# Kernel tuning notes

Measured on AMD Instinct MI355X. Metric: run time of the kernel, lower is better.

The kernel has to match this reference:

```python
import jax, jax.numpy as jnp
import numpy as np

NUM_HEAD = 16
EMBED_DIM = 1024
HEAD_DIM = EMBED_DIM // NUM_HEAD
QK_DIM = EMBED_DIM  # qk_dim defaults to embed_dim


def setup_inputs() -> dict:
    key = jax.random.key(0)
    k1, k2, k3 = jax.random.split(key, 3)
    x = jax.random.normal(k1, (4, 2048, EMBED_DIM), dtype=jnp.float32)
    # xavier_uniform-like init scale
    lim_qkv = float(np.sqrt(6.0 / (EMBED_DIM + 3 * EMBED_DIM)))
    lim_out = float(np.sqrt(6.0 / (EMBED_DIM + EMBED_DIM)))
    W_QKV = jax.random.uniform(k2, (EMBED_DIM, 3 * EMBED_DIM), jnp.float32, -lim_qkv, lim_qkv)
    W_Out = jax.random.uniform(k3, (EMBED_DIM, EMBED_DIM), jnp.float32, -lim_out, lim_out)
    return {"x": x, "W_QKV": W_QKV, "W_Out": W_Out}


def reference(x, W_QKV, W_Out):
    bsz, slen, _ = x.shape
    # [b,s,3E] -> [b,s,H,hd,3] -> [b,H,s,hd,3]  (interleaved qkv layout, as in torch source)
    qkv = (x @ W_QKV).reshape(bsz, slen, NUM_HEAD, HEAD_DIM, 3).transpose(0, 2, 1, 3, 4)
    q, k, v = qkv[..., 0], qkv[..., 1], qkv[..., 2]
    # NOTE: module scales by sqrt(qk_dim) (full dim), not sqrt(head_dim)
    scores = jnp.einsum("bhqd,bhkd->bhqk", q, k) / np.sqrt(QK_DIM).astype(np.float32)
    attn = jax.nn.softmax(scores, axis=-1)  # dropout p=0.0 -> identity
    out = jnp.einsum("bhqk,bhkd->bhqd", attn, v)  # [b,H,s,hd]
    out = out.transpose(0, 2, 1, 3).reshape(bsz, slen, EMBED_DIM)
    return out @ W_Out
```

## Files before the change

kernel.cpp:

```cpp
#include <hip/hip_runtime.h>
#include <stdint.h>

typedef __bf16 bf16x8 __attribute__((ext_vector_type(8)));
typedef float f32x4 __attribute__((ext_vector_type(4)));
typedef float f32x16 __attribute__((ext_vector_type(16)));
typedef unsigned short u16x8 __attribute__((ext_vector_type(8)));

#if __has_builtin(__builtin_amdgcn_mfma_f32_32x32x16_bf16)
#define MFMA32(a, b, c) __builtin_amdgcn_mfma_f32_32x32x16_bf16((a), (b), (c), 0, 0, 0)
#else
static __device__ __forceinline__ f32x16 MFMA32(bf16x8, bf16x8, f32x16 c) { return c; }
#endif

#if __has_builtin(__builtin_amdgcn_exp2f)
#define EXP2(x) __builtin_amdgcn_exp2f(x)
#else
#define EXP2(x) exp2f(x)
#endif

#if __has_builtin(__builtin_amdgcn_s_setprio)
#define SETPRIO(n) __builtin_amdgcn_s_setprio(n)
#else
#define SETPRIO(n)
#endif

__device__ __forceinline__ unsigned short f2bf(float f) {
    unsigned int u = __float_as_uint(f);
    u += 0x7fffu + ((u >> 16) & 1u);
    return (unsigned short)(u >> 16);
}

__device__ __forceinline__ int swz64(int row, int c) {
    return (c & 7) | ((((c >> 3) ^ row) & 7) << 3);
}

__device__ __forceinline__ int vperm32(int d, int s) {
    int c8 = ((s >> 5) << 2) | (((s >> 4) & 1) << 1) | ((s >> 2) & 1);
    int intra = (s & 3) | (((s >> 3) & 1) << 2);
    return intra + (((c8 ^ d) & 7) << 3);
}

__device__ __forceinline__ void glds16(const unsigned short* g, unsigned short* l) {
    __builtin_amdgcn_global_load_lds((const __attribute__((address_space(1))) void*)g,
                                     (__attribute__((address_space(3))) void*)l, 16, 0, 0);
}

__device__ __forceinline__ void transpose_body(const float* __restrict__ in,
                                               unsigned short* __restrict__ out,
                                               unsigned short (*tile)[33],
                                               int K, int N, int permute, int nb, int kb) {
    int tx = threadIdx.x & 31, ty = threadIdx.x >> 5;
    #pragma unroll
    for (int r = ty; r < 32; r += 8)
        tile[r][tx] = f2bf(in[(size_t)(kb + r) * N + nb + tx]);
    __syncthreads();
    #pragma unroll
    for (int r = ty; r < 32; r += 8) {
        int n_orig = nb + r, col = kb + tx;
        int row;
        if (permute) {
            int h = n_orig / 192, rem = n_orig - h * 192;
            int d = rem / 3, cc = rem - 3 * d;
            row = cc * 1024 + h * 64 + d;
        } else {
            row = n_orig;
        }
        out[(size_t)row * K + (col & ~63) + swz64(row, col & 63)] = tile[tx][r];
    }
}

__global__ __launch_bounds__(256) void preprocess_kernel(const float* __restrict__ x,
                                                         const float* __restrict__ wqkv,
                                                         const float* __restrict__ wout,
                                                         unsigned short* __restrict__ xb,
                                                         unsigned short* __restrict__ wqkvt,
                                                         unsigned short* __restrict__ woutt) {
    __shared__ unsigned short tile[32][33];
    int bid = blockIdx.x;
    if (bid < 4096) {
        size_t id = (size_t)bid * 256 + threadIdx.x;
        int row = (int)(id >> 7);
        int cid = (int)(id & 127);
        const float4* src = (const float4*)(x + id * 8);
        float4 a = src[0], b = src[1];
        u16x8 o;
        o[0] = f2bf(a.x); o[1] = f2bf(a.y); o[2] = f2bf(a.z); o[3] = f2bf(a.w);
        o[4] = f2bf(b.x); o[5] = f2bf(b.y); o[6] = f2bf(b.z); o[7] = f2bf(b.w);
        int group = cid >> 3, ch = cid & 7;
        *(u16x8*)(xb + (size_t)row * 1024 + group * 64 + (((ch ^ row) & 7) << 3)) = o;
    } else if (bid < 7168) {
        int idx = bid - 4096;
        transpose_body(wqkv, wqkvt, tile, 1024, 3072, 1, (idx % 96) * 32, (idx / 96) * 32);
    } else {
        int idx = bid - 7168;
        transpose_body(wout, woutt, tile, 1024, 1024, 0, (idx % 32) * 32, (idx / 32) * 32);
    }
}

__device__ __forceinline__ void gemm128_mainloop(const unsigned short* __restrict__ A,
                                                 const unsigned short* __restrict__ Bt,
                                                 f32x4 acc[4][4]) {
    __shared__ unsigned short smem[4 * 128 * 64];
    const int t = threadIdx.x, lane = t & 63, w = t >> 6;
    const int wm = w & 1, wn = w >> 1;
    const int r16 = lane & 15, quad = lane >> 4;
    const size_t mb = (size_t)blockIdx.y * 128, nb = (size_t)blockIdx.x * 128;

    const f32x4 zf = {0.f, 0.f, 0.f, 0.f};
    #pragma unroll
    for (int i = 0; i < 4; i++)
        #pragma unroll
        for (int j = 0; j < 4; j++) acc[i][j] = zf;

    int aoff[2], boff[2];
    #pragma unroll
    for (int kkh = 0; kkh < 2; kkh++) {
        int chunk = ((kkh * 4 + quad) ^ (r16 & 7)) << 3;
        aoff[kkh] = (wm * 64 + r16) * 64 + chunk;
        boff[kkh] = (wn * 64 + r16) * 64 + chunk;
    }

    const unsigned short* ap = A + (mb + w * 32 + (lane >> 3)) * 1024 + (lane & 7) * 8;
    const unsigned short* bp = Bt + (nb + w * 32 + (lane >> 3)) * 1024 + (lane & 7) * 8;
    unsigned short* al = smem + w * 2048;
    unsigned short* bl = smem + 16384 + w * 2048;
    auto stage = [&](int reg) {
        #pragma unroll
        for (int c = 0; c < 4; c++) {
            glds16(ap + c * 8192, al + reg * 8192 + c * 512);
            glds16(bp + c * 8192, bl + reg * 8192 + c * 512);
        }
        ap += 64;
        bp += 64;
    };

    auto body = [&](const unsigned short* as, const unsigned short* bs) {
        #pragma unroll
        for (int kkh = 0; kkh < 2; kkh++) {
            bf16x8 af[4], bfv[4];
            #pragma unroll
            for (int i = 0; i < 4; i++) af[i] = *(const bf16x8*)(as + i * 1024 + aoff[kkh]);
            #pragma unroll
            for (int j = 0; j < 4; j++) bfv[j] = *(const bf16x8*)(bs + j * 1024 + boff[kkh]);
            SETPRIO(1);
            #pragma unroll
            for (int i = 0; i < 4; i++)
                #pragma unroll
                for (int j = 0; j < 4; j++)
                    acc[i][j] =
                        __builtin_amdgcn_mfma_f32_16x16x32_bf16(af[i], bfv[j], acc[i][j], 0, 0, 0);
            SETPRIO(0);
        }
    };

    const unsigned short* A0 = smem;
    const unsigned short* A1 = smem + 8192;
    const unsigned short* B0 = smem + 16384;
    const unsigned short* B1 = smem + 24576;

    stage(0);
    #pragma unroll 1
    for (int j = 0; j < 7; j++) {
        __syncthreads();
        stage(1);
        body(A0, B0);
        __syncthreads();
        stage(0);
        body(A1, B1);
    }
    __syncthreads();
    stage(1);
    body(A0, B0);
    __syncthreads();
    body(A1, B1);
}

__global__ __launch_bounds__(256) void gemm_qkv_kernel(const unsigned short* __restrict__ A,
                                                       const unsigned short* __restrict__ Bt,
                                                       unsigned short* __restrict__ Qo,
                                                       unsigned short* __restrict__ Ko,
                                                       unsigned short* __restrict__ Vo) {
    f32x4 acc[4][4];
    gemm128_mainloop(A, Bt, acc);
    const int t = threadIdx.x, lane = t & 63, w = t >> 6;
    const int wm = w & 1, wn = w >> 1;
    const int c16 = lane & 15, quad = lane >> 4;
    const int mb = blockIdx.y * 128, nb = blockIdx.x * 128;
    const int cls = nb >> 10;
    const int hh = ((nb & 1023) >> 6) + wn;
    const float SCALE_Q = 1.4426950408889634f / 32.0f;
    #pragma unroll
    for (int i = 0; i < 4; i++) {
        #pragma unroll
        for (int r = 0; r < 4; r++) {
            int m = mb + wm * 64 + i * 16 + quad * 4 + r;
            int b = m >> 11, s = m & 2047;
            int bh = b * 16 + hh;
            #pragma unroll
            for (int j = 0; j < 4; j++) {
                int d = j * 16 + c16;
                float v = acc[i][j][r];
                if (cls == 0)
                    Qo[((size_t)bh * 2048 + s) * 64 + swz64(s, d)] = f2bf(v * SCALE_Q);
                else if (cls == 1)
                    Ko[((size_t)bh * 2048 + s) * 64 + swz64(s, d)] = f2bf(v);
                else
                    Vo[((size_t)bh * 64 + d) * 2048 + (s & ~63) + vperm32(d, s & 63)] = f2bf(v);
            }
        }
    }
}

__global__ __launch_bounds__(256) void gemm_out_kernel(const unsigned short* __restrict__ A,
                                                       const unsigned short* __restrict__ Bt,
                                                       float* __restrict__ C) {
    f32x4 acc[4][4];
    gemm128_mainloop(A, Bt, acc);
    const int t = threadIdx.x, lane = t & 63, w = t >> 6;
    const int wm = w & 1, wn = w >> 1;
    const int c16 = lane & 15, quad = lane >> 4;
    const int mb = blockIdx.y * 128, nb = blockIdx.x * 128;
    #pragma unroll
    for (int i = 0; i < 4; i++)
        #pragma unroll
        for (int j = 0; j < 4; j++)
            #pragma unroll
            for (int r = 0; r < 4; r++) {
                int m = mb + wm * 64 + i * 16 + quad * 4 + r;
                int n = nb + wn * 64 + j * 16 + c16;
                C[(size_t)m * 1024 + n] = acc[i][j][r];
            }
}

__global__ __launch_bounds__(256) void attn_kernel(const unsigned short* __restrict__ Qg,
                                                   const unsigned short* __restrict__ Kg,
                                                   const unsigned short* __restrict__ Vt,
                                                   unsigned short* __restrict__ O) {
    __shared__ unsigned short smem[4 * 64 * 64];
    unsigned short* K0 = smem;
    unsigned short* K1 = smem + 4096;
    unsigned short* V0 = smem + 8192;
    unsigned short* V1 = smem + 12288;
    const int t = threadIdx.x, lane = t & 63, w = t >> 6;
    const int l31 = lane & 31, h = lane >> 5;
    const int i_disp = blockIdx.y * 16 + blockIdx.x;
    const int bh = (i_disp & 7) + 8 * (i_disp >> 7);
    const int q0 = ((i_disp >> 3) & 15) * 128;

    int coff[4];
    #pragma unroll
    for (int i = 0; i < 4; i++)
        coff[i] = l31 * 64 + ((((2 * i + h) ^ l31) & 7) << 3);

    bf16x8 qf[4];
    {
        int row = q0 + w * 32 + l31;
        const unsigned short* qbase = Qg + ((size_t)bh * 2048 + row) * 64;
        #pragma unroll
        for (int step = 0; step < 4; step++)
            qf[step] = *(const bf16x8*)(qbase + ((((2 * step + h) ^ row) & 7) << 3));
    }

    const unsigned short* kgp =
        Kg + ((size_t)bh * 2048 + w * 16 + (lane >> 3)) * 64 + (lane & 7) * 8;
    const unsigned short* vgp =
        Vt + ((size_t)bh * 64 + w * 16 + (lane >> 3)) * 2048 + (lane & 7) * 8;
    unsigned short* kl = smem + (w * 16) * 64;
    auto stage = [&](int reg) {
        #pragma unroll
        for (int c = 0; c < 2; c++) {
            glds16(kgp + c * 512, kl + reg * 4096 + c * 512);
            glds16(vgp + c * 16384, kl + 8192 + reg * 4096 + c * 512);
        }
        kgp += 4096;
        vgp += 64;
    };

    const f32x16 z16 = {0.f, 0.f, 0.f, 0.f, 0.f, 0.f, 0.f, 0.f,
                        0.f, 0.f, 0.f, 0.f, 0.f, 0.f, 0.f, 0.f};
    f32x16 acc0 = z16, acc1 = z16;
    float den = 0.f;

    auto pv32 = [&](const f32x16& sg, const unsigned short* vs, int c0) {
        #pragma unroll
        for (int p = 0; p < 2; p++) {
            float e0 = EXP2(sg[8 * p + 0]);
            float e1 = EXP2(sg[8 * p + 1]);
            float e2 = EXP2(sg[8 * p + 2]);
            float e3 = EXP2(sg[8 * p + 3]);
            float e4 = EXP2(sg[8 * p + 4]);
            float e5 = EXP2(sg[8 * p + 5]);
            float e6 = EXP2(sg[8 * p + 6]);
            float e7 = EXP2(sg[8 * p + 7]);
            den += ((e0 + e1) + (e2 + e3)) + ((e4 + e5) + (e6 + e7));
            bf16x8 pb = {(__bf16)e0, (__bf16)e1, (__bf16)e2, (__bf16)e3,
                         (__bf16)e4, (__bf16)e5, (__bf16)e6, (__bf16)e7};
            bf16x8 vf0 = *(const bf16x8*)(vs + coff[c0 + p]);
            bf16x8 vf1 = *(const bf16x8*)(vs + 2048 + coff[c0 + p]);
            SETPRIO(1);
            acc0 = MFMA32(pb, vf0, acc0);
            acc1 = MFMA32(pb, vf1, acc1);
            SETPRIO(0);
        }
    };

    auto body = [&](const unsigned short* ks, const unsigned short* vs) {
        f32x16 s0, s1;
        {
            bf16x8 ka = *(const bf16x8*)(ks + coff[0]);
            bf16x8 kb = *(const bf16x8*)(ks + 2048 + coff[0]);
            SETPRIO(1);
            s0 = MFMA32(ka, qf[0], z16);
            s1 = MFMA32(kb, qf[0], z16);
            SETPRIO(0);
        }
        #pragma unroll
        for (int step = 1; step < 4; step++) {
            bf16x8 ka = *(const bf16x8*)(ks + coff[step]);
            bf16x8 kb = *(const bf16x8*)(ks + 2048 + coff[step]);
            SETPRIO(1);
            s0 = MFMA32(ka, qf[step], s0);
            s1 = MFMA32(kb, qf[step], s1);
            SETPRIO(0);
        }
        pv32(s0, vs, 0);
        pv32(s1, vs, 2);
    };

    stage(0);
    #pragma unroll 1
    for (int it2 = 0; it2 < 15; it2++) {
        __syncthreads();
        stage(1);
        body(K0, V0);
        __syncthreads();
        stage(0);
        body(K1, V1);
    }
    __syncthreads();
    stage(1);
    body(K0, V0);
    __syncthreads();
    body(K1, V1);

    den += __shfl_xor(den, 32);

    const int b = bh >> 4, hd = bh & 15;
    #pragma unroll
    for (int reg = 0; reg < 16; reg++) {
        int qrl = (reg & 3) + 8 * (reg >> 2) + 4 * h;
        float rd = 1.0f / __shfl(den, qrl);
        int srow = q0 + w * 32 + qrl;
        size_t base = ((size_t)b * 2048 + srow) * 1024 + hd * 64;
        O[base + swz64(srow, l31)] = f2bf(acc0[reg] * rd);
        O[base + swz64(srow, 32 + l31)] = f2bf(acc1[reg] * rd);
    }
}

extern "C" void kernel_launch(void* const* d_in, const int* in_sizes, int n_in,
                              void* d_out, int out_size, void* d_ws, size_t ws_size,
                              hipStream_t stream) {
    (void)in_sizes; (void)n_in; (void)out_size; (void)ws_size;
    const float* x = (const float*)d_in[0];
    const float* wqkv = (const float*)d_in[1];
    const float* wout = (const float*)d_in[2];
    float* out = (float*)d_out;

    const size_t SZ_X = 8388608;
    const size_t SZ_WQKV = 3145728;
    const size_t SZ_WOUT = 1048576;

    unsigned short* ws = (unsigned short*)d_ws;
    unsigned short* xb = ws;
    unsigned short* wqkvt = xb + SZ_X;
    unsigned short* woutt = wqkvt + SZ_WQKV;
    unsigned short* Qa = woutt + SZ_WOUT;
    unsigned short* Ka = Qa + SZ_X;
    unsigned short* Va = Ka + SZ_X;
    unsigned short* attn = Va + SZ_X;

    preprocess_kernel<<<8192, 256, 0, stream>>>(x, wqkv, wout, xb, wqkvt, woutt);
    gemm_qkv_kernel<<<dim3(24, 64), 256, 0, stream>>>(xb, wqkvt, Qa, Ka, Va);
    attn_kernel<<<dim3(16, 64), 256, 0, stream>>>(Qa, Ka, Va, attn);
    gemm_out_kernel<<<dim3(8, 64), 256, 0, stream>>>(attn, woutt, out);
}
```

Baseline: 270.0 us.

## Switch GEMMs to 32x32x16 MFMA tiles and add XCD-aware block remapping

Both projection GEMMs now compute each warp's 64x64 tile with four 32x32x16 bf16 MFMAs per k-step instead of sixteen 16x16x32 MFMAs. This halves the LDS fragment loads per k-step and uses the larger MFMA shape. The epilogues are rewritten for the 32x32 accumulator layout. A block-index remap spreads consecutive block IDs across the eight XCDs so that neighbouring tiles share L2. The remap assumes the grid sizes are multiples of eight.

```diff
diff --git a/kernel.cpp b/kernel.cpp
--- a/kernel.cpp
+++ b/kernel.cpp
@@ -43,6 +43,13 @@
 __device__ __forceinline__ void glds16(const unsigned short* g, unsigned short* l) {
     __builtin_amdgcn_global_load_lds((const __attribute__((address_space(1))) void*)g,
                                      (__attribute__((address_space(3))) void*)l, 16, 0, 0);
+}
+
+__device__ __forceinline__ void xcd_remap(int nx, int per, int& bx, int& by) {
+    int i = blockIdx.y * nx + blockIdx.x;
+    int j = (i & 7) * per + (i >> 3);
+    bx = j % nx;
+    by = j / nx;
 }
 
 __device__ __forceinline__ void transpose_body(const float* __restrict__ in,
@@ -99,26 +106,26 @@
 
 __device__ __forceinline__ void gemm128_mainloop(const unsigned short* __restrict__ A,
                                                  const unsigned short* __restrict__ Bt,
-                                                 f32x4 acc[4][4]) {
+                                                 int mbi, int nbi,
+                                                 f32x16 acc[2][2]) {
     __shared__ unsigned short smem[4 * 128 * 64];
     const int t = threadIdx.x, lane = t & 63, w = t >> 6;
     const int wm = w & 1, wn = w >> 1;
-    const int r16 = lane & 15, quad = lane >> 4;
-    const size_t mb = (size_t)blockIdx.y * 128, nb = (size_t)blockIdx.x * 128;
-
-    const f32x4 zf = {0.f, 0.f, 0.f, 0.f};
-    #pragma unroll
-    for (int i = 0; i < 4; i++)
-        #pragma unroll
-        for (int j = 0; j < 4; j++) acc[i][j] = zf;
-
-    int aoff[2], boff[2];
-    #pragma unroll
-    for (int kkh = 0; kkh < 2; kkh++) {
-        int chunk = ((kkh * 4 + quad) ^ (r16 & 7)) << 3;
-        aoff[kkh] = (wm * 64 + r16) * 64 + chunk;
-        boff[kkh] = (wn * 64 + r16) * 64 + chunk;
-    }
+    const int l31 = lane & 31, h = lane >> 5;
+    const size_t mb = (size_t)mbi, nb = (size_t)nbi;
+
+    const f32x16 z16 = {0.f, 0.f, 0.f, 0.f, 0.f, 0.f, 0.f, 0.f,
+                        0.f, 0.f, 0.f, 0.f, 0.f, 0.f, 0.f, 0.f};
+    #pragma unroll
+    for (int mt = 0; mt < 2; mt++)
+        #pragma unroll
+        for (int nt = 0; nt < 2; nt++) acc[mt][nt] = z16;
+
+    int coff[4];
+    #pragma unroll
+    for (int ks = 0; ks < 4; ks++)
+        coff[ks] = l31 * 64 + ((((2 * ks + h) ^ l31) & 7) << 3);
+    const int aw = wm * 4096, bw = wn * 4096;
 
     const unsigned short* ap = A + (mb + w * 32 + (lane >> 3)) * 1024 + (lane & 7) * 8;
     const unsigned short* bp = Bt + (nb + w * 32 + (lane >> 3)) * 1024 + (lane & 7) * 8;
@@ -136,19 +143,16 @@
 
     auto body = [&](const unsigned short* as, const unsigned short* bs) {
         #pragma unroll
-        for (int kkh = 0; kkh < 2; kkh++) {
-            bf16x8 af[4], bfv[4];
-            #pragma unroll
-            for (int i = 0; i < 4; i++) af[i] = *(const bf16x8*)(as + i * 1024 + aoff[kkh]);
-            #pragma unroll
-            for (int j = 0; j < 4; j++) bfv[j] = *(const bf16x8*)(bs + j * 1024 + boff[kkh]);
+        for (int ks = 0; ks < 4; ks++) {
+            bf16x8 a0 = *(const bf16x8*)(as + aw + coff[ks]);
+            bf16x8 a1 = *(const bf16x8*)(as + aw + 2048 + coff[ks]);
+            bf16x8 b0 = *(const bf16x8*)(bs + bw + coff[ks]);
+            bf16x8 b1 = *(const bf16x8*)(bs + bw + 2048 + coff[ks]);
             SETPRIO(1);
-            #pragma unroll
-            for (int i = 0; i < 4; i++)
-                #pragma unroll
-                for (int j = 0; j < 4; j++)
-                    acc[i][j] =
-                        __builtin_amdgcn_mfma_f32_16x16x32_bf16(af[i], bfv[j], acc[i][j], 0, 0, 0);
+            acc[0][0] = MFMA32(a0, b0, acc[0][0]);
+            acc[0][1] = MFMA32(a0, b1, acc[0][1]);
+            acc[1][0] = MFMA32(a1, b0, acc[1][0]);
+            acc[1][1] = MFMA32(a1, b1, acc[1][1]);
             SETPRIO(0);
         }
     };
@@ -180,26 +184,28 @@
                                                        unsigned short* __restrict__ Qo,
                                                        unsigned short* __restrict__ Ko,
                                                        unsigned short* __restrict__ Vo) {
-    f32x4 acc[4][4];
-    gemm128_mainloop(A, Bt, acc);
-    const int t = threadIdx.x, lane = t & 63, w = t >> 6;
+    int bx, by;
+    xcd_remap(24, 192, bx, by);
+    f32x16 acc[2][2];
+    gemm128_mainloop(A, Bt, by * 128, bx * 128, acc);
+    const int lane = threadIdx.x & 63, w = threadIdx.x >> 6;
     const int wm = w & 1, wn = w >> 1;
-    const int c16 = lane & 15, quad = lane >> 4;
-    const int mb = blockIdx.y * 128, nb = blockIdx.x * 128;
+    const int l31 = lane & 31, h = lane >> 5;
+    const int mb = by * 128, nb = bx * 128;
     const int cls = nb >> 10;
     const int hh = ((nb & 1023) >> 6) + wn;
     const float SCALE_Q = 1.4426950408889634f / 32.0f;
     #pragma unroll
-    for (int i = 0; i < 4; i++) {
-        #pragma unroll
-        for (int r = 0; r < 4; r++) {
-            int m = mb + wm * 64 + i * 16 + quad * 4 + r;
-            int b = m >> 11, s = m & 2047;
-            int bh = b * 16 + hh;
+    for (int mt = 0; mt < 2; mt++) {
+        #pragma unroll
+        for (int nt = 0; nt < 2; nt++) {
             #pragma unroll
-            for (int j = 0; j < 4; j++) {
-                int d = j * 16 + c16;
-                float v = acc[i][j][r];
+            for (int reg = 0; reg < 16; reg++) {
+                int m = mb + wm * 64 + mt * 32 + (reg & 3) + 8 * (reg >> 2) + 4 * h;
+                int b = m >> 11, s = m & 2047;
+                int bh = b * 16 + hh;
+                int d = nt * 32 + l31;
+                float v = acc[mt][nt][reg];
                 if (cls == 0)
                     Qo[((size_t)bh * 2048 + s) * 64 + swz64(s, d)] = f2bf(v * SCALE_Q);
                 else if (cls == 1)
@@ -214,21 +220,23 @@
 __global__ __launch_bounds__(256) void gemm_out_kernel(const unsigned short* __restrict__ A,
                                                        const unsigned short* __restrict__ Bt,
                                                        float* __restrict__ C) {
-    f32x4 acc[4][4];
-    gemm128_mainloop(A, Bt, acc);
-    const int t = threadIdx.x, lane = t & 63, w = t >> 6;
+    int bx, by;
+    xcd_remap(8, 64, bx, by);
+    f32x16 acc[2][2];
+    gemm128_mainloop(A, Bt, by * 128, bx * 128, acc);
+    const int lane = threadIdx.x & 63, w = threadIdx.x >> 6;
     const int wm = w & 1, wn = w >> 1;
-    const int c16 = lane & 15, quad = lane >> 4;
-    const int mb = blockIdx.y * 128, nb = blockIdx.x * 128;
-    #pragma unroll
-    for (int i = 0; i < 4; i++)
-        #pragma unroll
-        for (int j = 0; j < 4; j++)
+    const int l31 = lane & 31, h = lane >> 5;
+    const int mb = by * 128, nb = bx * 128;
+    #pragma unroll
+    for (int mt = 0; mt < 2; mt++)
+        #pragma unroll
+        for (int nt = 0; nt < 2; nt++)
             #pragma unroll
-            for (int r = 0; r < 4; r++) {
-                int m = mb + wm * 64 + i * 16 + quad * 4 + r;
-                int n = nb + wn * 64 + j * 16 + c16;
-                C[(size_t)m * 1024 + n] = acc[i][j][r];
+            for (int reg = 0; reg < 16; reg++) {
+                int m = mb + wm * 64 + mt * 32 + (reg & 3) + 8 * (reg >> 2) + 4 * h;
+                int n = nb + wn * 64 + nt * 32 + l31;
+                C[(size_t)m * 1024 + n] = acc[mt][nt][reg];
             }
 }
 
```

New measurement: 278.2 us. 1.03x slower.
